# Kernel tuning notes

Measured on AMD Instinct MI355X. Metric: run time of the kernel, lower is better.

Reference implementation:

```python
import jax, jax.numpy as jnp
from jax import lax
import numpy as np

DIM = 128    # block channel dim C
RESO = 56    # H = W = patches_resolution
HEADS = 4    # block num_heads (each branch uses HEADS//2)
SPLIT = 2    # split_size (stripe width)
MLP_RATIO = 4
BATCH = 32


def _ln(x, g, b, eps=1e-5):
    mu = jnp.mean(x, axis=-1, keepdims=True)
    var = jnp.mean(jnp.square(x - mu), axis=-1, keepdims=True)
    return (x - mu) * lax.rsqrt(var + eps) * g + b


def _lepe_attn(q, k, v, cw, cb, H, W, H_sp, W_sp, heads):
    # q,k,v: (B, L=H*W, C). Cross-shaped window attention with depthwise-conv LePE.
    B, L, C = q.shape
    hd = C // heads
    scale = hd ** -0.5
    nH, nW = H // H_sp, W // W_sp
    tok = H_sp * W_sp

    def to_win(t):  # im2cswin: (B,L,C) -> (B*nH*nW, heads, tok, hd)
        t = t.transpose(0, 2, 1).reshape(B, C, H, W)
        t = t.reshape(B, C, nH, H_sp, nW, W_sp).transpose(0, 2, 4, 3, 5, 1)
        return t.reshape(-1, tok, heads, hd).transpose(0, 2, 1, 3)

    qw = to_win(q) * scale
    kw = to_win(k)

    # v as per-window images (B*nW_total, C, H_sp, W_sp) for the depthwise conv LePE
    vimg = v.transpose(0, 2, 1).reshape(B, C, H, W)
    vimg = vimg.reshape(B, C, nH, H_sp, nW, W_sp).transpose(0, 2, 4, 1, 3, 5).reshape(-1, C, H_sp, W_sp)
    lepe = lax.conv_general_dilated(vimg, cw, (1, 1), 'SAME', feature_group_count=C,
                                    dimension_numbers=('NCHW', 'OIHW', 'NCHW')) + cb[None, :, None, None]
    lepe = lepe.reshape(-1, heads, hd, tok).transpose(0, 1, 3, 2)  # (W', heads, tok, hd)
    vw = vimg.reshape(-1, heads, hd, tok).transpose(0, 1, 3, 2)

    attn = jax.nn.softmax(jnp.einsum('whqd,whkd->whqk', qw, kw), axis=-1)
    out = jnp.einsum('whqk,whkd->whqd', attn, vw) + lepe        # (W', heads, tok, hd)
    out = out.transpose(0, 2, 1, 3).reshape(-1, tok, C)
    # windows2img -> (B, H*W, C)
    out = out.reshape(B, nH, nW, H_sp, W_sp, C).transpose(0, 1, 3, 2, 4, 5).reshape(B, H * W, C)
    return out


def setup_inputs() -> dict:
    key = jax.random.key(0)
    ks = jax.random.split(key, 12)
    B, L, C = BATCH, RESO * RESO, DIM
    Ch = C // 2
    Hid = C * MLP_RATIO
    s = 0.02
    f32 = jnp.float32
    return {
        'x':       jax.random.normal(ks[0], (B, L, C), f32),
        'norm1_g': jnp.ones((C,), f32), 'norm1_b': jnp.zeros((C,), f32),
        'qkv_w':   jax.random.normal(ks[1], (C, 3 * C), f32) * s,
        'proj_w':  jax.random.normal(ks[2], (C, C), f32) * s,
        'proj_b':  jnp.zeros((C,), f32),
        'conv_w0': jax.random.normal(ks[3], (Ch, 1, 3, 3), f32) * s,
        'conv_b0': jnp.zeros((Ch,), f32),
        'conv_w1': jax.random.normal(ks[4], (Ch, 1, 3, 3), f32) * s,
        'conv_b1': jnp.zeros((Ch,), f32),
        'norm2_g': jnp.ones((C,), f32), 'norm2_b': jnp.zeros((C,), f32),
        'fc1_w':   jax.random.normal(ks[5], (C, Hid), f32) * s,
        'fc1_b':   jnp.zeros((Hid,), f32),
        'fc2_w':   jax.random.normal(ks[6], (Hid, C), f32) * s,
        'fc2_b':   jnp.zeros((C,), f32),
    }


def reference(x, norm1_g, norm1_b, qkv_w, proj_w, proj_b, conv_w0, conv_b0,
              conv_w1, conv_b1, norm2_g, norm2_b, fc1_w, fc1_b, fc2_w, fc2_b):
    B, L, C = x.shape
    H = W = RESO
    Ch = C // 2
    h = HEADS // 2

    img = _ln(x, norm1_g, norm1_b)
    qkv = (img @ qkv_w).reshape(B, L, 3, C)
    q, k, v = qkv[:, :, 0], qkv[:, :, 1], qkv[:, :, 2]

    # branch 0 (idx=0): H_sp = reso, W_sp = split  |  branch 1 (idx=1): H_sp = split, W_sp = reso
    x1 = _lepe_attn(q[..., :Ch], k[..., :Ch], v[..., :Ch], conv_w0, conv_b0, H, W, H, SPLIT, h)
    x2 = _lepe_attn(q[..., Ch:], k[..., Ch:], v[..., Ch:], conv_w1, conv_b1, H, W, SPLIT, W, h)

    att = jnp.concatenate([x1, x2], axis=2) @ proj_w + proj_b
    x = x + att
    y = _ln(x, norm2_g, norm2_b)
    y = jax.nn.gelu(y @ fc1_w + fc1_b, approximate=False) @ fc2_w + fc2_b
    return x + y
```

## Files before the change

### kernel.cpp

```cpp
#include <hip/hip_runtime.h>
#include <hip/hip_bf16.h>
#include <math.h>

#define NTOK 100352
typedef __attribute__((ext_vector_type(8))) short short8_t;
typedef __attribute__((ext_vector_type(4))) float f32x4;

union I4S8 { int4 i; short h[8]; short8_t v; };

__device__ __forceinline__ short f2bf(float f) {
    union { float f; unsigned u; } x; x.f = f;
    unsigned r = x.u + 0x7FFFu + ((x.u >> 16) & 1u);
    return (short)(r >> 16);
}
__device__ __forceinline__ float bf2f(short s) {
    union { unsigned u; float f; } x; x.u = ((unsigned)(unsigned short)s) << 16;
    return x.f;
}

#define GLDS16(gsrc, ldst) __builtin_amdgcn_global_load_lds( \
    (const __attribute__((address_space(1))) unsigned int*)(gsrc), \
    (__attribute__((address_space(3))) unsigned int*)(ldst), 16, 0, 0)

__global__ void prep_weights(const float* __restrict__ qkv_w, const float* __restrict__ proj_w,
                             const float* __restrict__ fc1_w, const float* __restrict__ fc2_w,
                             short* __restrict__ wt) {
    int idx = blockIdx.x * 256 + threadIdx.x;
    const float* src; int K, N, base;
    if (idx < 49152)       { src = qkv_w;  K = 128; N = 384; base = 0; }
    else if (idx < 65536)  { src = proj_w; K = 128; N = 128; base = 49152; }
    else if (idx < 131072) { src = fc1_w;  K = 128; N = 512; base = 65536; }
    else                   { src = fc2_w;  K = 512; N = 128; base = 131072; }
    int local = idx - base;
    int n = local / K, k = local - n * K;
    wt[idx] = f2bf(src[k * N + n]);
}

__global__ __launch_bounds__(256) void ln_kernel(const float* __restrict__ in,
                                                 const float* __restrict__ g,
                                                 const float* __restrict__ b,
                                                 short* __restrict__ out) {
    int token = blockIdx.x * 4 + (threadIdx.x >> 6);
    int lane = threadIdx.x & 63;
    const float2 v = *reinterpret_cast<const float2*>(in + (size_t)token * 128 + lane * 2);
    float s = v.x + v.y;
    float sq = v.x * v.x + v.y * v.y;
    #pragma unroll
    for (int m = 32; m >= 1; m >>= 1) {
        s  += __shfl_xor(s, m);
        sq += __shfl_xor(sq, m);
    }
    float mean = s * (1.0f / 128.0f);
    float var = sq * (1.0f / 128.0f) - mean * mean;
    float rstd = rsqrtf(var + 1e-5f);
    float2 gg = *reinterpret_cast<const float2*>(g + lane * 2);
    float2 bb = *reinterpret_cast<const float2*>(b + lane * 2);
    float o0 = (v.x - mean) * rstd * gg.x + bb.x;
    float o1 = (v.y - mean) * rstd * gg.y + bb.y;
    unsigned pack = ((unsigned)(unsigned short)f2bf(o0)) |
                    (((unsigned)(unsigned short)f2bf(o1)) << 16);
    *reinterpret_cast<unsigned*>(out + (size_t)token * 128 + lane * 2) = pack;
}

template<int EPI>
__global__ __launch_bounds__(256) void gemm_kernel(const short* __restrict__ A,
                                                   const short* __restrict__ BT,
                                                   const float* __restrict__ bias,
                                                   const float* __restrict__ res,
                                                   void* __restrict__ out,
                                                   int N, int K) {
    __shared__ short As[128 * 64];
    const int m0 = blockIdx.x * 128;
    const int n0 = blockIdx.y * 128;
    const int tid = threadIdx.x;
    const int w = tid >> 6, lane = tid & 63;
    const int wr = w >> 1, wc = w & 1;
    const int r = lane & 15, g = lane >> 4;

    f32x4 acc[4][4];
    #pragma unroll
    for (int i = 0; i < 4; ++i)
        #pragma unroll
        for (int j = 0; j < 4; ++j) acc[i][j] = (f32x4){0.f, 0.f, 0.f, 0.f};

    const int srow_in_issue = lane >> 3;
    const int sseg_lane = lane & 7;

    for (int kc = 0; kc < K; kc += 64) {
        #pragma unroll
        for (int t = 0; t < 4; ++t) {
            int row = w * 32 + t * 8 + srow_in_issue;
            int sseg = sseg_lane ^ (row & 7);
            const short* gsrc = A + (size_t)(m0 + row) * K + kc + sseg * 8;
            GLDS16(gsrc, &As[(w * 32 + t * 8) * 64]);
        }
        short8_t bfr[2][4];
        #pragma unroll
        for (int ks = 0; ks < 2; ++ks)
            #pragma unroll
            for (int nf = 0; nf < 4; ++nf) {
                int brow = n0 + wc * 64 + nf * 16 + r;
                bfr[ks][nf] = *reinterpret_cast<const short8_t*>(
                    BT + (size_t)brow * K + kc + ks * 32 + g * 8);
            }
        __syncthreads();
        #pragma unroll
        for (int ks = 0; ks < 2; ++ks) {
            #pragma unroll
            for (int mf = 0; mf < 4; ++mf) {
                int arow = wr * 64 + mf * 16 + r;
                int s0 = (ks * 4 + g) ^ (arow & 7);
                short8_t af = *reinterpret_cast<const short8_t*>(&As[arow * 64 + s0 * 8]);
                #pragma unroll
                for (int nf = 0; nf < 4; ++nf)
                    acc[mf][nf] = __builtin_amdgcn_mfma_f32_16x16x32_bf16(af, bfr[ks][nf], acc[mf][nf], 0, 0, 0);
            }
        }
        __syncthreads();
    }

    #pragma unroll
    for (int nf = 0; nf < 4; ++nf) {
        int col = n0 + wc * 64 + nf * 16 + r;
        float bv = (EPI != 0) ? bias[col] : 0.f;
        #pragma unroll
        for (int mf = 0; mf < 4; ++mf) {
            #pragma unroll
            for (int j = 0; j < 4; ++j) {
                int row = m0 + wr * 64 + mf * 16 + g * 4 + j;
                float v = acc[mf][nf][j];
                if (EPI == 0) {
                    ((short*)out)[(size_t)row * N + col] = f2bf(v);
                } else if (EPI == 1) {
                    ((float*)out)[(size_t)row * N + col] = v + bv + res[(size_t)row * N + col];
                } else {
                    float t = v + bv;
                    float ge = 0.5f * t * (1.0f + erff(t * 0.70710678118654752f));
                    ((short*)out)[(size_t)row * N + col] = f2bf(ge);
                }
            }
        }
    }
}

__global__ __launch_bounds__(256) void attn_kernel(const short* __restrict__ qkv,
                                                   const float* __restrict__ cw0,
                                                   const float* __restrict__ cb0,
                                                   const float* __restrict__ cw1,
                                                   const float* __restrict__ cb1,
                                                   short* __restrict__ attout) {
    __shared__ short P[112][120];
    __shared__ short vT[32][120];

    const int win = blockIdx.x;
    const int head = blockIdx.y;
    const int type = blockIdx.z;
    const int b = win / 28;
    const int wdx = win - b * 28;
    const int tid = threadIdx.x;
    const int wv = tid >> 6, lane = tid & 63;
    const int r = lane & 15, g = lane >> 4;
    const int chb = type * 64 + head * 32;
    const float* cw = type ? cw1 : cw0;
    const float* cb = type ? cb1 : cb0;

    auto rowof = [&](int t) -> int {
        int l;
        if (type == 0) { int hs = t >> 1, wsp = t & 1; l = hs * 56 + wdx * 2 + wsp; }
        else           { int hs = (t >= 56) ? 1 : 0, wsp = t - hs * 56; l = (wdx * 2 + hs) * 56 + wsp; }
        return b * 3136 + l;
    };

    for (int i = tid; i < 448; i += 256) {
        int tt = i >> 2, seg = i & 3;
        int roww = rowof(tt);
        I4S8 u; u.i = *reinterpret_cast<const int4*>(qkv + (size_t)roww * 384 + 256 + chb + seg * 8);
        #pragma unroll
        for (int j = 0; j < 8; ++j) vT[seg * 8 + j][tt] = u.h[j];
    }

    short8_t kf[7];
    #pragma unroll
    for (int nt = 0; nt < 7; ++nt) {
        int roww = rowof(nt * 16 + r);
        kf[nt] = *reinterpret_cast<const short8_t*>(qkv + (size_t)roww * 384 + 128 + chb + g * 8);
    }

    f32x4 sa[2][7];
    #pragma unroll
    for (int t = 0; t < 2; ++t)
        #pragma unroll
        for (int nt = 0; nt < 7; ++nt)
            sa[t][nt] = (f32x4){0.f, 0.f, 0.f, 0.f};

    #pragma unroll
    for (int t = 0; t < 2; ++t) {
        int mt = wv + 4 * t;
        if (mt < 7) {
            int roww = rowof(mt * 16 + r);
            short8_t af = *reinterpret_cast<const short8_t*>(qkv + (size_t)roww * 384 + chb + g * 8);
            #pragma unroll
            for (int nt = 0; nt < 7; ++nt)
                sa[t][nt] = __builtin_amdgcn_mfma_f32_16x16x32_bf16(af, kf[nt], sa[t][nt], 0, 0, 0);
        }
    }

    const float scale = 0.17677669529663687f;
    #pragma unroll
    for (int t = 0; t < 2; ++t) {
        int mt = wv + 4 * t;
        if (mt < 7) {
            #pragma unroll
            for (int j = 0; j < 4; ++j) {
                float sv[7];
                float mx = -1e30f;
                #pragma unroll
                for (int nt = 0; nt < 7; ++nt) { sv[nt] = sa[t][nt][j] * scale; mx = fmaxf(mx, sv[nt]); }
                #pragma unroll
                for (int m = 8; m >= 1; m >>= 1) mx = fmaxf(mx, __shfl_xor(mx, m));
                float sum = 0.f;
                #pragma unroll
                for (int nt = 0; nt < 7; ++nt) { sv[nt] = __expf(sv[nt] - mx); sum += sv[nt]; }
                #pragma unroll
                for (int m = 8; m >= 1; m >>= 1) sum += __shfl_xor(sum, m);
                float inv = 1.0f / sum;
                int row = mt * 16 + g * 4 + j;
                #pragma unroll
                for (int nt = 0; nt < 7; ++nt)
                    P[row][nt * 16 + r] = f2bf(sv[nt] * inv);
            }
        }
    }
    __syncthreads();

    #pragma unroll
    for (int t = 0; t < 4; ++t) {
        int idx = wv + 4 * t;
        if (idx < 14) {
            int mt = idx >> 1, nt = idx & 1;
            int m0 = mt * 16, n0 = nt * 16;
            f32x4 acc = {0.f, 0.f, 0.f, 0.f};
            #pragma unroll
            for (int ks = 0; ks < 4; ++ks) {
                short8_t pa, vb;
                if (ks < 3 || g < 2) {
                    int k0 = ks * 32 + g * 8;
                    pa = *reinterpret_cast<const short8_t*>(&P[m0 + r][k0]);
                    vb = *reinterpret_cast<const short8_t*>(&vT[n0 + r][k0]);
                } else {
                    #pragma unroll
                    for (int j = 0; j < 8; ++j) { pa[j] = 0; vb[j] = 0; }
                }
                acc = __builtin_amdgcn_mfma_f32_16x16x32_bf16(pa, vb, acc, 0, 0, 0);
            }
            int d = n0 + r;
            int cl = head * 32 + d;
            float w9[9];
            #pragma unroll
            for (int j = 0; j < 9; ++j) w9[j] = cw[cl * 9 + j];
            float cbias = cb[cl];
            #pragma unroll
            for (int j = 0; j < 4; ++j) {
                int tok = m0 + g * 4 + j;
                float v = acc[j];
                int hs, wsp;
                if (type == 0) { hs = tok >> 1; wsp = tok & 1; }
                else           { hs = (tok >= 56) ? 1 : 0; wsp = tok - hs * 56; }
                float lp = cbias;
                #pragma unroll
                for (int ky = 0; ky < 3; ++ky) {
                    int hh = hs + ky - 1;
                    bool okh = (type == 0) ? (hh >= 0 && hh < 56) : (hh >= 0 && hh < 2);
                    #pragma unroll
                    for (int kx = 0; kx < 3; ++kx) {
                        int wwp = wsp + kx - 1;
                        bool okw = (type == 0) ? (wwp >= 0 && wwp < 2) : (wwp >= 0 && wwp < 56);
                        if (okh && okw) {
                            int tt = (type == 0) ? (hh * 2 + wwp) : (hh * 56 + wwp);
                            lp += w9[ky * 3 + kx] * bf2f(vT[d][tt]);
                        }
                    }
                }
                v += lp;
                int roww = rowof(tok);
                attout[(size_t)roww * 128 + chb + d] = f2bf(v);
            }
        }
    }
}

extern "C" void kernel_launch(void* const* d_in, const int* in_sizes, int n_in,
                              void* d_out, int out_size, void* d_ws, size_t ws_size,
                              hipStream_t stream) {
    const float* x      = (const float*)d_in[0];
    const float* n1g    = (const float*)d_in[1];
    const float* n1b    = (const float*)d_in[2];
    const float* qkv_w  = (const float*)d_in[3];
    const float* proj_w = (const float*)d_in[4];
    const float* proj_b = (const float*)d_in[5];
    const float* cw0    = (const float*)d_in[6];
    const float* cb0    = (const float*)d_in[7];
    const float* cw1    = (const float*)d_in[8];
    const float* cb1    = (const float*)d_in[9];
    const float* n2g    = (const float*)d_in[10];
    const float* n2b    = (const float*)d_in[11];
    const float* fc1_w  = (const float*)d_in[12];
    const float* fc1_b  = (const float*)d_in[13];
    const float* fc2_w  = (const float*)d_in[14];
    const float* fc2_b  = (const float*)d_in[15];
    float* out = (float*)d_out;
    char* ws = (char*)d_ws;

    short* img   = (short*)(ws + 0);
    short* qkv   = (short*)(ws + 25690112);
    short* att   = (short*)(ws + 102760448);
    float* xres  = (float*)(ws + 128450560);
    short* wT    = (short*)(ws + 179830784);
    short* wqkvT  = wT;
    short* wprojT = wT + 49152;
    short* wfc1T  = wT + 65536;
    short* wfc2T  = wT + 131072;
    short* hidden = qkv;
    short* y2     = img;

    prep_weights<<<768, 256, 0, stream>>>(qkv_w, proj_w, fc1_w, fc2_w, wT);
    ln_kernel<<<25088, 256, 0, stream>>>(x, n1g, n1b, img);
    gemm_kernel<0><<<dim3(784, 3), 256, 0, stream>>>(img, wqkvT, nullptr, nullptr, qkv, 384, 128);
    attn_kernel<<<dim3(896, 2, 2), 256, 0, stream>>>(qkv, cw0, cb0, cw1, cb1, att);
    gemm_kernel<1><<<dim3(784, 1), 256, 0, stream>>>(att, wprojT, proj_b, x, xres, 128, 128);
    ln_kernel<<<25088, 256, 0, stream>>>(xres, n2g, n2b, y2);
    gemm_kernel<2><<<dim3(784, 4), 256, 0, stream>>>(y2, wfc1T, fc1_b, nullptr, hidden, 512, 128);
    gemm_kernel<1><<<dim3(784, 1), 256, 0, stream>>>(hidden, wfc2T, fc2_b, xres, out, 128, 512);
}
```

Before: 401.1 us.

## Fuse LayerNorm2 into proj GEMM and fuse fc1+GELU+fc2 into one MLP kernel

```diff
diff --git a/kernel.cpp b/kernel.cpp
--- a/kernel.cpp
+++ b/kernel.cpp
@@ -16,6 +16,9 @@
 __device__ __forceinline__ float bf2f(short s) {
     union { unsigned u; float f; } x; x.u = ((unsigned)(unsigned short)s) << 16;
     return x.f;
+}
+__device__ __forceinline__ unsigned pk2(float a, float b) {
+    return ((unsigned)(unsigned short)f2bf(a)) | (((unsigned)(unsigned short)f2bf(b)) << 16);
 }
 
 #define GLDS16(gsrc, ldst) __builtin_amdgcn_global_load_lds( \
@@ -63,82 +66,217 @@
 }
 
 template<int EPI>
-__global__ __launch_bounds__(256) void gemm_kernel(const short* __restrict__ A,
-                                                   const short* __restrict__ BT,
-                                                   const float* __restrict__ bias,
-                                                   const float* __restrict__ res,
-                                                   void* __restrict__ out,
-                                                   int N, int K) {
-    __shared__ short As[128 * 64];
+__global__ __launch_bounds__(256) void gemm128(const short* __restrict__ A,
+                                               const short* __restrict__ BT,
+                                               const float* __restrict__ bias,
+                                               const float* __restrict__ resid,
+                                               const float* __restrict__ g2,
+                                               const float* __restrict__ b2,
+                                               short* __restrict__ outb,
+                                               float* __restrict__ outf,
+                                               int N) {
+    __shared__ short As[128 * 128];
+    __shared__ short Bs[128 * 128];
     const int m0 = blockIdx.x * 128;
     const int n0 = blockIdx.y * 128;
     const int tid = threadIdx.x;
     const int w = tid >> 6, lane = tid & 63;
-    const int wr = w >> 1, wc = w & 1;
     const int r = lane & 15, g = lane >> 4;
-
-    f32x4 acc[4][4];
-    #pragma unroll
-    for (int i = 0; i < 4; ++i)
-        #pragma unroll
-        for (int j = 0; j < 4; ++j) acc[i][j] = (f32x4){0.f, 0.f, 0.f, 0.f};
-
-    const int srow_in_issue = lane >> 3;
-    const int sseg_lane = lane & 7;
-
-    for (int kc = 0; kc < K; kc += 64) {
-        #pragma unroll
-        for (int t = 0; t < 4; ++t) {
-            int row = w * 32 + t * 8 + srow_in_issue;
-            int sseg = sseg_lane ^ (row & 7);
-            const short* gsrc = A + (size_t)(m0 + row) * K + kc + sseg * 8;
-            GLDS16(gsrc, &As[(w * 32 + t * 8) * 64]);
-        }
-        short8_t bfr[2][4];
-        #pragma unroll
-        for (int ks = 0; ks < 2; ++ks)
-            #pragma unroll
-            for (int nf = 0; nf < 4; ++nf) {
-                int brow = n0 + wc * 64 + nf * 16 + r;
-                bfr[ks][nf] = *reinterpret_cast<const short8_t*>(
-                    BT + (size_t)brow * K + kc + ks * 32 + g * 8);
-            }
-        __syncthreads();
-        #pragma unroll
-        for (int ks = 0; ks < 2; ++ks) {
-            #pragma unroll
-            for (int mf = 0; mf < 4; ++mf) {
-                int arow = wr * 64 + mf * 16 + r;
-                int s0 = (ks * 4 + g) ^ (arow & 7);
-                short8_t af = *reinterpret_cast<const short8_t*>(&As[arow * 64 + s0 * 8]);
-                #pragma unroll
-                for (int nf = 0; nf < 4; ++nf)
-                    acc[mf][nf] = __builtin_amdgcn_mfma_f32_16x16x32_bf16(af, bfr[ks][nf], acc[mf][nf], 0, 0, 0);
-            }
-        }
-        __syncthreads();
-    }
-
-    #pragma unroll
-    for (int nf = 0; nf < 4; ++nf) {
-        int col = n0 + wc * 64 + nf * 16 + r;
-        float bv = (EPI != 0) ? bias[col] : 0.f;
+    const int rr = lane >> 4, ss = lane & 15;
+
+    #pragma unroll
+    for (int t = 0; t < 8; ++t) {
+        int row = w * 32 + t * 4 + rr;
+        int sseg = (ss & 8) | ((ss ^ row) & 7);
+        GLDS16(A  + (size_t)(m0 + row) * 128 + sseg * 8, &As[(w * 32 + t * 4) * 128]);
+        GLDS16(BT + (size_t)(n0 + row) * 128 + sseg * 8, &Bs[(w * 32 + t * 4) * 128]);
+    }
+    __syncthreads();
+
+    f32x4 acc[2][8];
+    #pragma unroll
+    for (int mf = 0; mf < 2; ++mf)
+        #pragma unroll
+        for (int nt = 0; nt < 8; ++nt) acc[mf][nt] = (f32x4){0.f, 0.f, 0.f, 0.f};
+
+    #pragma unroll
+    for (int kf = 0; kf < 4; ++kf) {
+        const int q = kf * 4 + g;
+        short8_t bfr[8], af[2];
+        #pragma unroll
+        for (int nt = 0; nt < 8; ++nt) {
+            int row = nt * 16 + r;
+            int seg = (q & 8) | ((q ^ row) & 7);
+            bfr[nt] = *reinterpret_cast<const short8_t*>(&Bs[row * 128 + seg * 8]);
+        }
+        #pragma unroll
+        for (int mf = 0; mf < 2; ++mf) {
+            int row = w * 32 + mf * 16 + r;
+            int seg = (q & 8) | ((q ^ row) & 7);
+            af[mf] = *reinterpret_cast<const short8_t*>(&As[row * 128 + seg * 8]);
+        }
+        #pragma unroll
+        for (int mf = 0; mf < 2; ++mf)
+            #pragma unroll
+            for (int nt = 0; nt < 8; ++nt)
+                acc[mf][nt] = __builtin_amdgcn_mfma_f32_16x16x32_bf16(bfr[nt], af[mf], acc[mf][nt], 0, 0, 0);
+    }
+
+    if (EPI == 0) {
+        #pragma unroll
+        for (int mf = 0; mf < 2; ++mf) {
+            int row = m0 + w * 32 + mf * 16 + r;
+            #pragma unroll
+            for (int nt = 0; nt < 8; ++nt) {
+                int col = n0 + nt * 16 + g * 4;
+                uint2 p;
+                p.x = pk2(acc[mf][nt][0], acc[mf][nt][1]);
+                p.y = pk2(acc[mf][nt][2], acc[mf][nt][3]);
+                *reinterpret_cast<uint2*>(&outb[(size_t)row * N + col]) = p;
+            }
+        }
+    } else {
+        #pragma unroll
+        for (int mf = 0; mf < 2; ++mf) {
+            int row = m0 + w * 32 + mf * 16 + r;
+            float s = 0.f, sq = 0.f;
+            #pragma unroll
+            for (int nt = 0; nt < 8; ++nt) {
+                int col = nt * 16 + g * 4;
+                f32x4 b4 = *reinterpret_cast<const f32x4*>(&bias[col]);
+                f32x4 x4 = *reinterpret_cast<const f32x4*>(&resid[(size_t)row * 128 + col]);
+                #pragma unroll
+                for (int j = 0; j < 4; ++j) {
+                    float v = acc[mf][nt][j] + b4[j] + x4[j];
+                    acc[mf][nt][j] = v;
+                    s += v; sq += v * v;
+                }
+                *reinterpret_cast<f32x4*>(&outf[(size_t)row * 128 + col]) = acc[mf][nt];
+            }
+            s  += __shfl_xor(s, 16);  s  += __shfl_xor(s, 32);
+            sq += __shfl_xor(sq, 16); sq += __shfl_xor(sq, 32);
+            float mean = s * (1.0f / 128.0f);
+            float var = sq * (1.0f / 128.0f) - mean * mean;
+            float rstd = rsqrtf(var + 1e-5f);
+            #pragma unroll
+            for (int nt = 0; nt < 8; ++nt) {
+                int col = nt * 16 + g * 4;
+                f32x4 g4  = *reinterpret_cast<const f32x4*>(&g2[col]);
+                f32x4 bb4 = *reinterpret_cast<const f32x4*>(&b2[col]);
+                float y0 = (acc[mf][nt][0] - mean) * rstd * g4[0] + bb4[0];
+                float y1 = (acc[mf][nt][1] - mean) * rstd * g4[1] + bb4[1];
+                float y2v = (acc[mf][nt][2] - mean) * rstd * g4[2] + bb4[2];
+                float y3 = (acc[mf][nt][3] - mean) * rstd * g4[3] + bb4[3];
+                uint2 p; p.x = pk2(y0, y1); p.y = pk2(y2v, y3);
+                *reinterpret_cast<uint2*>(&outb[(size_t)row * 128 + col]) = p;
+            }
+        }
+    }
+}
+
+__global__ __launch_bounds__(256) void mlp_kernel(const short* __restrict__ Y,
+                                                  const short* __restrict__ W1T,
+                                                  const float* __restrict__ b1,
+                                                  const short* __restrict__ W2T,
+                                                  const float* __restrict__ b2,
+                                                  const float* __restrict__ xres,
+                                                  float* __restrict__ out) {
+    __shared__ short hid[64 * 512];
+    const int m0 = blockIdx.x * 64;
+    const int tid = threadIdx.x;
+    const int w = tid >> 6, lane = tid & 63;
+    const int r = lane & 15, g = lane >> 4;
+
+    short8_t af[4][4];
+    #pragma unroll
+    for (int mf = 0; mf < 4; ++mf)
+        #pragma unroll
+        for (int kf = 0; kf < 4; ++kf)
+            af[mf][kf] = *reinterpret_cast<const short8_t*>(
+                &Y[(size_t)(m0 + mf * 16 + r) * 128 + kf * 32 + g * 8]);
+
+    #pragma unroll
+    for (int np = 0; np < 2; ++np) {
+        f32x4 acc[4][4];
+        #pragma unroll
+        for (int mf = 0; mf < 4; ++mf)
+            #pragma unroll
+            for (int nt = 0; nt < 4; ++nt) acc[mf][nt] = (f32x4){0.f, 0.f, 0.f, 0.f};
+        #pragma unroll
+        for (int kf = 0; kf < 4; ++kf) {
+            short8_t bfr[4];
+            #pragma unroll
+            for (int nt = 0; nt < 4; ++nt) {
+                int hc = w * 128 + np * 64 + nt * 16 + r;
+                bfr[nt] = *reinterpret_cast<const short8_t*>(&W1T[(size_t)hc * 128 + kf * 32 + g * 8]);
+            }
+            #pragma unroll
+            for (int mf = 0; mf < 4; ++mf)
+                #pragma unroll
+                for (int nt = 0; nt < 4; ++nt)
+                    acc[mf][nt] = __builtin_amdgcn_mfma_f32_16x16x32_bf16(bfr[nt], af[mf][kf], acc[mf][nt], 0, 0, 0);
+        }
         #pragma unroll
         for (int mf = 0; mf < 4; ++mf) {
-            #pragma unroll
-            for (int j = 0; j < 4; ++j) {
-                int row = m0 + wr * 64 + mf * 16 + g * 4 + j;
-                float v = acc[mf][nf][j];
-                if (EPI == 0) {
-                    ((short*)out)[(size_t)row * N + col] = f2bf(v);
-                } else if (EPI == 1) {
-                    ((float*)out)[(size_t)row * N + col] = v + bv + res[(size_t)row * N + col];
-                } else {
-                    float t = v + bv;
-                    float ge = 0.5f * t * (1.0f + erff(t * 0.70710678118654752f));
-                    ((short*)out)[(size_t)row * N + col] = f2bf(ge);
+            int row = mf * 16 + r;
+            #pragma unroll
+            for (int nt = 0; nt < 4; ++nt) {
+                int col = w * 128 + np * 64 + nt * 16 + g * 4;
+                f32x4 b4 = *reinterpret_cast<const f32x4*>(&b1[col]);
+                float h[4];
+                #pragma unroll
+                for (int j = 0; j < 4; ++j) {
+                    float t = acc[mf][nt][j] + b4[j];
+                    h[j] = 0.5f * t * (1.0f + erff(t * 0.70710678118654752f));
                 }
-            }
+                int s16 = col >> 3;
+                int half = (col >> 2) & 1;
+                int seg = (s16 & 56) | ((s16 ^ row) & 7);
+                uint2 p; p.x = pk2(h[0], h[1]); p.y = pk2(h[2], h[3]);
+                *reinterpret_cast<uint2*>((char*)hid + row * 1024 + seg * 16 + half * 8) = p;
+            }
+        }
+    }
+    __syncthreads();
+
+    f32x4 acc2[4][2];
+    #pragma unroll
+    for (int tt = 0; tt < 4; ++tt)
+        #pragma unroll
+        for (int o = 0; o < 2; ++o) acc2[tt][o] = (f32x4){0.f, 0.f, 0.f, 0.f};
+    #pragma unroll
+    for (int kf = 0; kf < 16; ++kf) {
+        const int q = kf * 4 + g;
+        short8_t bfr2[2], hf[4];
+        #pragma unroll
+        for (int o = 0; o < 2; ++o) {
+            int ocol = w * 32 + o * 16 + r;
+            bfr2[o] = *reinterpret_cast<const short8_t*>(&W2T[(size_t)ocol * 512 + kf * 32 + g * 8]);
+        }
+        #pragma unroll
+        for (int tt = 0; tt < 4; ++tt) {
+            int row = tt * 16 + r;
+            int seg = (q & 56) | ((q ^ row) & 7);
+            hf[tt] = *reinterpret_cast<const short8_t*>((char*)hid + row * 1024 + seg * 16);
+        }
+        #pragma unroll
+        for (int tt = 0; tt < 4; ++tt)
+            #pragma unroll
+            for (int o = 0; o < 2; ++o)
+                acc2[tt][o] = __builtin_amdgcn_mfma_f32_16x16x32_bf16(bfr2[o], hf[tt], acc2[tt][o], 0, 0, 0);
+    }
+    #pragma unroll
+    for (int tt = 0; tt < 4; ++tt) {
+        int row = m0 + tt * 16 + r;
+        #pragma unroll
+        for (int o = 0; o < 2; ++o) {
+            int col = w * 32 + o * 16 + g * 4;
+            f32x4 b4 = *reinterpret_cast<const f32x4*>(&b2[col]);
+            f32x4 x4 = *reinterpret_cast<const f32x4*>(&xres[(size_t)row * 128 + col]);
+            f32x4 v;
+            #pragma unroll
+            for (int j = 0; j < 4; ++j) v[j] = acc2[tt][o][j] + b4[j] + x4[j];
+            *reinterpret_cast<f32x4*>(&out[(size_t)row * 128 + col]) = v;
         }
     }
 }
@@ -320,15 +458,14 @@
     short* wprojT = wT + 49152;
     short* wfc1T  = wT + 65536;
     short* wfc2T  = wT + 131072;
-    short* hidden = qkv;
     short* y2     = img;
 
     prep_weights<<<768, 256, 0, stream>>>(qkv_w, proj_w, fc1_w, fc2_w, wT);
     ln_kernel<<<25088, 256, 0, stream>>>(x, n1g, n1b, img);
-    gemm_kernel<0><<<dim3(784, 3), 256, 0, stream>>>(img, wqkvT, nullptr, nullptr, qkv, 384, 128);
+    gemm128<0><<<dim3(784, 3), 256, 0, stream>>>(img, wqkvT, nullptr, nullptr, nullptr, nullptr,
+                                                 qkv, nullptr, 384);
     attn_kernel<<<dim3(896, 2, 2), 256, 0, stream>>>(qkv, cw0, cb0, cw1, cb1, att);
-    gemm_kernel<1><<<dim3(784, 1), 256, 0, stream>>>(att, wprojT, proj_b, x, xres, 128, 128);
-    ln_kernel<<<25088, 256, 0, stream>>>(xres, n2g, n2b, y2);
-    gemm_kernel<2><<<dim3(784, 4), 256, 0, stream>>>(y2, wfc1T, fc1_b, nullptr, hidden, 512, 128);
-    gemm_kernel<1><<<dim3(784, 1), 256, 0, stream>>>(hidden, wfc2T, fc2_b, xres, out, 128, 512);
-}
+    gemm128<1><<<dim3(784, 1), 256, 0, stream>>>(att, wprojT, proj_b, x, n2g, n2b,
+                                                 y2, xres, 128);
+    mlp_kernel<<<1568, 256, 0, stream>>>(y2, wfc1T, fc1_b, wfc2T, fc2_b, xres, out);
+}
```

New measurement: 397.0 us. About the same (-1.0%).
